# Optimization experiments

Hardware: AMD Instinct MI355X
Metric: run time of the kernel (lower is better)

## Reference

```python
import jax, jax.numpy as jnp
import numpy as np

FP8_MAX = 448.0  # max finite value of float8_e4m3fn


def setup_inputs() -> dict:
    key = jax.random.key(0)
    k1, k2, k3 = jax.random.split(key, 3)
    B, S, D_IN, D_OUT = 2, 4096, 2048, 8192
    x = jax.random.normal(k1, (B, S, D_IN), dtype=jnp.float32)
    # Weight is stored pre-quantized in fp8 (per-tensor scale), layout (in, out)
    w_fp32 = jax.random.normal(k2, (D_IN, D_OUT), dtype=jnp.float32) * 0.02
    weight_scale = jnp.float32(jnp.max(jnp.abs(w_fp32)) / FP8_MAX)
    weight = jnp.clip(w_fp32 / weight_scale, -FP8_MAX, FP8_MAX).astype(jnp.float8_e4m3fn)
    input_scale = jnp.float32(0.05)  # static per-tensor activation scale
    bias = jax.random.normal(k3, (D_OUT,), dtype=jnp.float32)
    return {"x": x, "weight": weight, "weight_scale": weight_scale,
            "input_scale": input_scale, "bias": bias}


def reference(x, weight, weight_scale, input_scale, bias):
    # static_quantize_e4m3_per_tensor: q = cast_fp8(clip(x / s)), returns (q, s)
    q = jnp.clip(x / input_scale, -FP8_MAX, FP8_MAX).astype(jnp.float8_e4m3fn)
    q2d = q.reshape(-1, q.shape[-1]).astype(jnp.float32)  # [B*S, D_in]
    w = weight.astype(jnp.float32)                         # [D_in, D_out]
    # cublas_scaled_mm: (q @ w) * scale_a * scale_b, out in x.dtype
    out = jnp.matmul(q2d, w) * (input_scale * weight_scale)
    out = out.astype(x.dtype) + bias.astype(x.dtype)
    return out.reshape(x.shape[:-1] + (out.shape[-1],))
```

## Files before the change

kernel.cpp:

```cpp
#include <hip/hip_runtime.h>

typedef __attribute__((ext_vector_type(4))) float floatx4;
typedef __attribute__((ext_vector_type(8))) int   intx8;

__device__ __forceinline__ unsigned int pack4_fp8(float f0, float f1, float f2, float f3) {
    int v = __builtin_amdgcn_cvt_pk_fp8_f32(f0, f1, 0, false);
    v = __builtin_amdgcn_cvt_pk_fp8_f32(f2, f3, v, true);
    return (unsigned int)v;
}

__device__ __forceinline__ void gload16(const unsigned char* g, unsigned char* l) {
    __builtin_amdgcn_global_load_lds(
        (const __attribute__((address_space(1))) unsigned int*)g,
        (__attribute__((address_space(3))) unsigned int*)l, 16, 0, 0);
}

__global__ void detect_kernel(const unsigned int* __restrict__ W, int* __restrict__ flag) {
    __shared__ int ok[2];
    if (threadIdx.x == 0) { ok[0] = 1; ok[1] = 1; }
    __syncthreads();
    int f32ok = 1, bf16ok = 1;
#pragma unroll
    for (int i = 0; i < 16; ++i) {
        unsigned int w = W[threadIdx.x * 16 + i];
        if (w & 0x000FFFFFu) f32ok = 0;
        if (w & 0x000F000Fu) bf16ok = 0;
    }
    if (!f32ok)  atomicAnd(&ok[0], 0);
    if (!bf16ok) atomicAnd(&ok[1], 0);
    __syncthreads();
    if (threadIdx.x == 0) *flag = ok[0] ? 2 : (ok[1] ? 1 : 0);
}

__global__ void quant_kernel(const float* __restrict__ x,
                             unsigned int* __restrict__ q,
                             const float* __restrict__ iscale, int n8) {
    int i = blockIdx.x * blockDim.x + threadIdx.x;
    if (i >= n8) return;
    float s = iscale[0];
    const float4* xv = (const float4*)x;
    float4 a = xv[2 * i];
    float4 b = xv[2 * i + 1];
    float v[8] = {a.x, a.y, a.z, a.w, b.x, b.y, b.z, b.w};
#pragma unroll
    for (int j = 0; j < 8; ++j) {
        float t = v[j] / s;
        v[j] = fminf(fmaxf(t, -448.0f), 448.0f);
    }
    q[2 * i]     = pack4_fp8(v[0], v[1], v[2], v[3]);
    q[2 * i + 1] = pack4_fp8(v[4], v[5], v[6], v[7]);
}

template <int MODE>
__device__ __forceinline__ void ingest_body(const unsigned char* __restrict__ W,
                                            unsigned char* __restrict__ Wt,
                                            int K, int N,
                                            unsigned char (*tile)[68]) {
    const int k0 = blockIdx.y * 64;
    const int n0 = blockIdx.x * 64;
    const int t = threadIdx.x;
    const int kr = t >> 2;
    const int cg = (t & 3) * 16;
    const size_t eidx = (size_t)(k0 + kr) * N + (n0 + cg);

    unsigned int w4[4];
    if constexpr (MODE == 0) {
        uint4 v = *(const uint4*)(W + eidx);
        w4[0] = v.x; w4[1] = v.y; w4[2] = v.z; w4[3] = v.w;
    } else if constexpr (MODE == 1) {
        const uint4* p = (const uint4*)((const unsigned short*)W + eidx);
        uint4 A0 = p[0], A1 = p[1];
        unsigned int uw[8] = {A0.x, A0.y, A0.z, A0.w, A1.x, A1.y, A1.z, A1.w};
#pragma unroll
        for (int g = 0; g < 4; ++g) {
            float f0 = __uint_as_float((uw[2 * g] & 0xFFFFu) << 16);
            float f1 = __uint_as_float((uw[2 * g] >> 16) << 16);
            float f2 = __uint_as_float((uw[2 * g + 1] & 0xFFFFu) << 16);
            float f3 = __uint_as_float((uw[2 * g + 1] >> 16) << 16);
            w4[g] = pack4_fp8(f0, f1, f2, f3);
        }
    } else {
        const float4* p = (const float4*)((const float*)W + eidx);
#pragma unroll
        for (int g = 0; g < 4; ++g) {
            float4 f = p[g];
            w4[g] = pack4_fp8(f.x, f.y, f.z, f.w);
        }
    }
#pragma unroll
    for (int g = 0; g < 4; ++g)
        *(unsigned int*)&tile[kr][cg + 4 * g] = w4[g];
    __syncthreads();

    const int nr = t >> 2;
    const int kg = (t & 3) * 16;
    uint4 o;
    unsigned int w[4];
#pragma unroll
    for (int g = 0; g < 4; ++g) {
        unsigned int b0 = tile[kg + g * 4 + 0][nr];
        unsigned int b1 = tile[kg + g * 4 + 1][nr];
        unsigned int b2 = tile[kg + g * 4 + 2][nr];
        unsigned int b3 = tile[kg + g * 4 + 3][nr];
        w[g] = b0 | (b1 << 8) | (b2 << 16) | (b3 << 24);
    }
    o.x = w[0]; o.y = w[1]; o.z = w[2]; o.w = w[3];
    *(uint4*)(Wt + (size_t)(n0 + nr) * K + k0 + kg) = o;
}

__global__ void ingest_kernel(const unsigned char* __restrict__ W,
                              unsigned char* __restrict__ Wt,
                              const int* __restrict__ flag, int K, int N) {
    __shared__ __align__(16) unsigned char tile[64][68];
    const int mode = *flag;
    if (mode == 0)      ingest_body<0>(W, Wt, K, N, tile);
    else if (mode == 1) ingest_body<1>(W, Wt, K, N, tile);
    else                ingest_body<2>(W, Wt, K, N, tile);
}

__global__ __launch_bounds__(512, 2) void gemm_mxfp8_kernel(
    const unsigned char* __restrict__ A,
    const unsigned char* __restrict__ Bt,
    float* __restrict__ C,
    const float* __restrict__ bias,
    const float* __restrict__ wscale,
    const float* __restrict__ iscale,
    int M, int N, int K) {
    __shared__ __align__(16) unsigned char As[2 * 32768];
    __shared__ __align__(16) unsigned char Bs[2 * 32768];

    const int tid  = threadIdx.x;
    const int lane = tid & 63;
    const int wv   = tid >> 6;
    const int wm   = wv >> 2;
    const int wn   = wv & 3;
    const int r16  = lane & 15;
    const int cq   = lane >> 4;

    const int bm = blockIdx.y * 256;
    const int bn = blockIdx.x * 256;

    const unsigned char* ga[4];
    const unsigned char* gb[4];
    int lo[4];
#pragma unroll
    for (int j = 0; j < 4; ++j) {
        const int u   = wv * 4 + j;
        const int rb  = u >> 1;
        const int rg  = u & 1;
        const int row = rb * 16 + r16;
        const int col = cq * 32 + rg * 16;
        ga[j] = A  + (size_t)(bm + row) * K + col;
        gb[j] = Bt + (size_t)(bn + row) * K + col;
        lo[j] = u * 1024;
    }

    floatx4 acc[8][4] = {};
    const int NT = K >> 7;

#pragma unroll
    for (int j = 0; j < 4; ++j) {
        gload16(ga[j], &As[lo[j]]);
        gload16(gb[j], &Bs[lo[j]]);
        ga[j] += 128; gb[j] += 128;
    }
    if (NT > 1) {
#pragma unroll
        for (int j = 0; j < 4; ++j) {
            gload16(gb[j], &Bs[32768 + lo[j]]);
            gb[j] += 128;
        }
        asm volatile("s_waitcnt vmcnt(4)" ::: "memory");
    } else {
        asm volatile("s_waitcnt vmcnt(0)" ::: "memory");
    }
    __builtin_amdgcn_s_barrier();
    __builtin_amdgcn_sched_barrier(0);

    union U8 { intx8 v; uint4 q[2]; };

#define READ_FRAG(dst, base, blk)                                   \
    do {                                                            \
        U8 _u;                                                      \
        const unsigned char* _p = (base) + (blk) * 2048 + lane * 16;\
        _u.q[0] = *(const uint4*)_p;                                \
        _u.q[1] = *(const uint4*)(_p + 1024);                       \
        (dst) = _u.v;                                               \
    } while (0)

#define MFMA8(a0, a1, i0, i1)                                               \
    do {                                                                    \
        __builtin_amdgcn_s_setprio(1);                                      \
        _Pragma("unroll")                                                   \
        for (int j = 0; j < 4; ++j)                                         \
            acc[i0][j] = __builtin_amdgcn_mfma_scale_f32_16x16x128_f8f6f4(  \
                a0, bf[j], acc[i0][j], 0, 0, 0, 0x7F7F7F7F, 0, 0x7F7F7F7F); \
        _Pragma("unroll")                                                   \
        for (int j = 0; j < 4; ++j)                                         \
            acc[i1][j] = __builtin_amdgcn_mfma_scale_f32_16x16x128_f8f6f4(  \
                a1, bf[j], acc[i1][j], 0, 0, 0, 0x7F7F7F7F, 0, 0x7F7F7F7F); \
        __builtin_amdgcn_s_setprio(0);                                      \
    } while (0)

#define PHASE_WAIT()                                             \
    do {                                                         \
        __builtin_amdgcn_s_barrier();                            \
        asm volatile("s_waitcnt lgkmcnt(0)" ::: "memory");       \
        __builtin_amdgcn_sched_barrier(0);                       \
    } while (0)

    for (int kt = 0; kt < NT; ++kt) {
        const unsigned char* Ab = &As[(kt & 1) * 32768];
        const unsigned char* Bb = &Bs[(kt & 1) * 32768];
        unsigned char* An  = &As[((kt + 1) & 1) * 32768];
        unsigned char* Bn2 = &Bs[(kt & 1) * 32768];
        const bool pfA = (kt + 1 < NT);
        const bool pfB = (kt + 2 < NT);

        intx8 bf[4], afa, afb;
        READ_FRAG(bf[0], Bb, wn * 4 + 0);
        READ_FRAG(bf[1], Bb, wn * 4 + 1);
        READ_FRAG(bf[2], Bb, wn * 4 + 2);
        READ_FRAG(bf[3], Bb, wn * 4 + 3);
        READ_FRAG(afa, Ab, wm * 8 + 0);
        READ_FRAG(afb, Ab, wm * 8 + 1);
        if (pfA) {
            gload16(ga[0], An + lo[0]); gload16(ga[1], An + lo[1]);
            ga[0] += 128; ga[1] += 128;
        }
        PHASE_WAIT();
        MFMA8(afa, afb, 0, 1);
        __builtin_amdgcn_s_barrier();

        READ_FRAG(afa, Ab, wm * 8 + 2);
        READ_FRAG(afb, Ab, wm * 8 + 3);
        if (pfA) {
            gload16(ga[2], An + lo[2]); gload16(ga[3], An + lo[3]);
            ga[2] += 128; ga[3] += 128;
        }
        PHASE_WAIT();
        MFMA8(afa, afb, 2, 3);
        __builtin_amdgcn_s_barrier();

        READ_FRAG(afa, Ab, wm * 8 + 4);
        READ_FRAG(afb, Ab, wm * 8 + 5);
        if (pfB) {
            gload16(gb[0], Bn2 + lo[0]); gload16(gb[1], Bn2 + lo[1]);
            gb[0] += 128; gb[1] += 128;
        }
        PHASE_WAIT();
        MFMA8(afa, afb, 4, 5);
        __builtin_amdgcn_s_barrier();

        READ_FRAG(afa, Ab, wm * 8 + 6);
        READ_FRAG(afb, Ab, wm * 8 + 7);
        if (pfB) {
            gload16(gb[2], Bn2 + lo[2]); gload16(gb[3], Bn2 + lo[3]);
            gb[2] += 128; gb[3] += 128;
        }
        PHASE_WAIT();
        MFMA8(afa, afb, 6, 7);
        if (pfB) {
            asm volatile("s_waitcnt vmcnt(4)" ::: "memory");
        } else {
            asm volatile("s_waitcnt vmcnt(0)" ::: "memory");
        }
        __builtin_amdgcn_s_barrier();
        __builtin_amdgcn_sched_barrier(0);
    }
    (void)M;
#undef READ_FRAG
#undef MFMA8
#undef PHASE_WAIT

    const float scale = iscale[0] * wscale[0];
    const int row0 = bm + wm * 128 + (cq << 2);
    const int col0 = bn + wn * 64 + r16;
#pragma unroll
    for (int j = 0; j < 4; ++j) {
        const int col = col0 + j * 16;
        const float bv = bias[col];
#pragma unroll
        for (int i = 0; i < 8; ++i) {
            const int row = row0 + i * 16;
            float* cp = C + (size_t)row * N + col;
#pragma unroll
            for (int r = 0; r < 4; ++r)
                cp[(size_t)r * N] = acc[i][j][r] * scale + bv;
        }
    }
}

extern "C" void kernel_launch(void* const* d_in, const int* in_sizes, int n_in,
                              void* d_out, int out_size, void* d_ws, size_t ws_size,
                              hipStream_t stream) {
    const float* x          = (const float*)d_in[0];
    const unsigned char* w  = (const unsigned char*)d_in[1];
    const float* wscale     = (const float*)d_in[2];
    const float* iscale     = (const float*)d_in[3];
    const float* bias       = (const float*)d_in[4];
    float* out              = (float*)d_out;

    const int D_OUT = in_sizes[4];
    const int D_IN  = in_sizes[1] / D_OUT;
    const int M     = in_sizes[0] / D_IN;

    int* flag         = (int*)d_ws;
    unsigned char* q  = (unsigned char*)d_ws + 256;
    unsigned char* wt = q + (size_t)M * D_IN;

    detect_kernel<<<1, 256, 0, stream>>>((const unsigned int*)w, flag);
    const int n8 = (M * D_IN) / 8;
    quant_kernel<<<(n8 + 255) / 256, 256, 0, stream>>>(x, (unsigned int*)q, iscale, n8);
    dim3 tg(D_OUT / 64, D_IN / 64);
    ingest_kernel<<<tg, 256, 0, stream>>>(w, wt, flag, D_IN, D_OUT);
    gemm_mxfp8_kernel<<<dim3(D_OUT / 256, M / 256), 512, 0, stream>>>(
        q, wt, out, bias, wscale, iscale, M, D_OUT, D_IN);
}
```

Baseline: 549.8 us.

## Switch GEMM inner loop from 16x16x128 to 32x32x64 scaled FP8 MFMA

Replaces the 16x16x128 scaled MFMA tiles with 32x32x64 tiles. Each wave now holds 4x2 floatx16 accumulators instead of 8x4 floatx4, and the LDS fragment addressing and K-splitting across phases are remapped to the 32x32 operand layout. The epilogue is rewritten for the 32x32 output lane mapping. The aim is fewer MFMA issues and fewer LDS fragment reads per tile, in exchange for a different LDS read pattern that may cause bank conflicts and a write pattern with less coalescing.

```diff
diff --git a/kernel.cpp b/kernel.cpp
--- a/kernel.cpp
+++ b/kernel.cpp
@@ -1,7 +1,8 @@
 #include <hip/hip_runtime.h>
 
-typedef __attribute__((ext_vector_type(4))) float floatx4;
-typedef __attribute__((ext_vector_type(8))) int   intx8;
+typedef __attribute__((ext_vector_type(4)))  float floatx4;
+typedef __attribute__((ext_vector_type(16))) float floatx16;
+typedef __attribute__((ext_vector_type(8)))  int   intx8;
 
 __device__ __forceinline__ unsigned int pack4_fp8(float f0, float f1, float f2, float f3) {
     int v = __builtin_amdgcn_cvt_pk_fp8_f32(f0, f1, 0, false);
@@ -155,8 +156,10 @@
         lo[j] = u * 1024;
     }
 
-    floatx4 acc[8][4] = {};
+    floatx16 acc[4][2] = {};
     const int NT = K >> 7;
+
+    const int labase = ((lane >> 4) & 1) * 2048 + (lane & 15) * 16 + (lane >> 5) * 256;
 
 #pragma unroll
     for (int j = 0; j < 4; ++j) {
@@ -179,26 +182,25 @@
 
     union U8 { intx8 v; uint4 q[2]; };
 
-#define READ_FRAG(dst, base, blk)                                   \
+#define READ_FRAG(dst, p)                                           \
     do {                                                            \
         U8 _u;                                                      \
-        const unsigned char* _p = (base) + (blk) * 2048 + lane * 16;\
-        _u.q[0] = *(const uint4*)_p;                                \
-        _u.q[1] = *(const uint4*)(_p + 1024);                       \
+        _u.q[0] = *(const uint4*)(p);                               \
+        _u.q[1] = *(const uint4*)((p) + 1024);                      \
         (dst) = _u.v;                                               \
     } while (0)
 
-#define MFMA8(a0, a1, i0, i1)                                               \
+#define MFMA4(afA, afB, mA, mB, b0_, b1_)                                   \
     do {                                                                    \
         __builtin_amdgcn_s_setprio(1);                                      \
-        _Pragma("unroll")                                                   \
-        for (int j = 0; j < 4; ++j)                                         \
-            acc[i0][j] = __builtin_amdgcn_mfma_scale_f32_16x16x128_f8f6f4(  \
-                a0, bf[j], acc[i0][j], 0, 0, 0, 0x7F7F7F7F, 0, 0x7F7F7F7F); \
-        _Pragma("unroll")                                                   \
-        for (int j = 0; j < 4; ++j)                                         \
-            acc[i1][j] = __builtin_amdgcn_mfma_scale_f32_16x16x128_f8f6f4(  \
-                a1, bf[j], acc[i1][j], 0, 0, 0, 0x7F7F7F7F, 0, 0x7F7F7F7F); \
+        acc[mA][0] = __builtin_amdgcn_mfma_scale_f32_32x32x64_f8f6f4(       \
+            afA, b0_, acc[mA][0], 0, 0, 0, 0x7F7F7F7F, 0, 0x7F7F7F7F);      \
+        acc[mA][1] = __builtin_amdgcn_mfma_scale_f32_32x32x64_f8f6f4(       \
+            afA, b1_, acc[mA][1], 0, 0, 0, 0x7F7F7F7F, 0, 0x7F7F7F7F);      \
+        acc[mB][0] = __builtin_amdgcn_mfma_scale_f32_32x32x64_f8f6f4(       \
+            afB, b0_, acc[mB][0], 0, 0, 0, 0x7F7F7F7F, 0, 0x7F7F7F7F);      \
+        acc[mB][1] = __builtin_amdgcn_mfma_scale_f32_32x32x64_f8f6f4(       \
+            afB, b1_, acc[mB][1], 0, 0, 0, 0x7F7F7F7F, 0, 0x7F7F7F7F);      \
         __builtin_amdgcn_s_setprio(0);                                      \
     } while (0)
 
@@ -217,49 +219,52 @@
         const bool pfA = (kt + 1 < NT);
         const bool pfB = (kt + 2 < NT);
 
-        intx8 bf[4], afa, afb;
-        READ_FRAG(bf[0], Bb, wn * 4 + 0);
-        READ_FRAG(bf[1], Bb, wn * 4 + 1);
-        READ_FRAG(bf[2], Bb, wn * 4 + 2);
-        READ_FRAG(bf[3], Bb, wn * 4 + 3);
-        READ_FRAG(afa, Ab, wm * 8 + 0);
-        READ_FRAG(afb, Ab, wm * 8 + 1);
+        const unsigned char* aB = Ab + labase;
+        const unsigned char* bB = Bb + labase;
+        intx8 b00, b01, b10, b11, af0, af1;
+
+        READ_FRAG(b00, bB + (wn * 4 + 0) * 2048);
+        READ_FRAG(b01, bB + (wn * 4 + 2) * 2048);
+        READ_FRAG(af0, aB + (wm * 8 + 0) * 2048);
+        READ_FRAG(af1, aB + (wm * 8 + 2) * 2048);
         if (pfA) {
             gload16(ga[0], An + lo[0]); gload16(ga[1], An + lo[1]);
             ga[0] += 128; ga[1] += 128;
         }
         PHASE_WAIT();
-        MFMA8(afa, afb, 0, 1);
+        MFMA4(af0, af1, 0, 1, b00, b01);
         __builtin_amdgcn_s_barrier();
 
-        READ_FRAG(afa, Ab, wm * 8 + 2);
-        READ_FRAG(afb, Ab, wm * 8 + 3);
+        READ_FRAG(b10, bB + (wn * 4 + 0) * 2048 + 512);
+        READ_FRAG(b11, bB + (wn * 4 + 2) * 2048 + 512);
+        READ_FRAG(af0, aB + (wm * 8 + 4) * 2048);
+        READ_FRAG(af1, aB + (wm * 8 + 6) * 2048);
         if (pfA) {
             gload16(ga[2], An + lo[2]); gload16(ga[3], An + lo[3]);
             ga[2] += 128; ga[3] += 128;
         }
         PHASE_WAIT();
-        MFMA8(afa, afb, 2, 3);
+        MFMA4(af0, af1, 2, 3, b00, b01);
         __builtin_amdgcn_s_barrier();
 
-        READ_FRAG(afa, Ab, wm * 8 + 4);
-        READ_FRAG(afb, Ab, wm * 8 + 5);
+        READ_FRAG(af0, aB + (wm * 8 + 0) * 2048 + 512);
+        READ_FRAG(af1, aB + (wm * 8 + 2) * 2048 + 512);
         if (pfB) {
             gload16(gb[0], Bn2 + lo[0]); gload16(gb[1], Bn2 + lo[1]);
             gb[0] += 128; gb[1] += 128;
         }
         PHASE_WAIT();
-        MFMA8(afa, afb, 4, 5);
+        MFMA4(af0, af1, 0, 1, b10, b11);
         __builtin_amdgcn_s_barrier();
 
-        READ_FRAG(afa, Ab, wm * 8 + 6);
-        READ_FRAG(afb, Ab, wm * 8 + 7);
+        READ_FRAG(af0, aB + (wm * 8 + 4) * 2048 + 512);
+        READ_FRAG(af1, aB + (wm * 8 + 6) * 2048 + 512);
         if (pfB) {
             gload16(gb[2], Bn2 + lo[2]); gload16(gb[3], Bn2 + lo[3]);
             gb[2] += 128; gb[3] += 128;
         }
         PHASE_WAIT();
-        MFMA8(afa, afb, 6, 7);
+        MFMA4(af0, af1, 2, 3, b10, b11);
         if (pfB) {
             asm volatile("s_waitcnt vmcnt(4)" ::: "memory");
         } else {
@@ -268,25 +273,24 @@
         __builtin_amdgcn_s_barrier();
         __builtin_amdgcn_sched_barrier(0);
     }
-    (void)M;
+    (void)M; (void)r16; (void)cq;
 #undef READ_FRAG
-#undef MFMA8
+#undef MFMA4
 #undef PHASE_WAIT
 
     const float scale = iscale[0] * wscale[0];
-    const int row0 = bm + wm * 128 + (cq << 2);
-    const int col0 = bn + wn * 64 + r16;
-#pragma unroll
-    for (int j = 0; j < 4; ++j) {
-        const int col = col0 + j * 16;
-        const float bv = bias[col];
-#pragma unroll
-        for (int i = 0; i < 8; ++i) {
-            const int row = row0 + i * 16;
-            float* cp = C + (size_t)row * N + col;
-#pragma unroll
-            for (int r = 0; r < 4; ++r)
-                cp[(size_t)r * N] = acc[i][j][r] * scale + bv;
+    const int colb = bn + wn * 64 + (lane & 31);
+    const float bv0 = bias[colb];
+    const float bv1 = bias[colb + 32];
+    const int rowb = bm + wm * 128 + 4 * (lane >> 5);
+#pragma unroll
+    for (int mb = 0; mb < 4; ++mb) {
+#pragma unroll
+        for (int r = 0; r < 16; ++r) {
+            const int row = rowb + mb * 32 + (r & 3) + 8 * (r >> 2);
+            float* cp = C + (size_t)row * N + colb;
+            cp[0]  = acc[mb][0][r] * scale + bv0;
+            cp[32] = acc[mb][1][r] * scale + bv1;
         }
     }
 }
```

New measurement: 507.4 us. -7.7%, faster.
